# Optimization experiments

Hardware: AMD Instinct MI355X
Metric: run time of the kernel (lower is better)

The kernel has to match this reference:

```python
import jax, jax.numpy as jnp
import numpy as np

B, S, D, E, K = 4, 4096, 1024, 8, 2


def setup_inputs() -> dict:
    key = jax.random.key(0)
    k0, k1, k2 = jax.random.split(key, 3)
    return {
        "x": jax.random.normal(k0, (B, S, D), dtype=jnp.float32),
        "gate_w": jax.random.normal(k1, (E, D), dtype=jnp.float32) * 0.02,   # torch Linear weight [out,in]
        "gate_b": jnp.zeros((E,), dtype=jnp.float32),
        "expert_w": jax.random.normal(k2, (E, D, D), dtype=jnp.float32) * 0.02,  # [E, out, in]
        "expert_b": jnp.zeros((E, D), dtype=jnp.float32),
    }


def reference(x, gate_w, gate_b, expert_w, expert_b):
    b, s, d = x.shape
    h = x.reshape(-1, d)                                   # [T, D], T = b*s
    # Router: gate linear -> softmax (float32) -> top-k -> renormalize
    router_logits = h @ gate_w.T + gate_b                  # [T, E]
    probs = jax.nn.softmax(router_logits.astype(jnp.float32), axis=-1)
    router_weights, selected_experts = jax.lax.top_k(probs, K)  # [T, K]
    router_weights = router_weights / router_weights.sum(axis=-1, keepdims=True)
    router_weights = router_weights.astype(h.dtype)
    # Combine weights per (token, expert): sum of top-k weights routed to each expert
    cw = (jax.nn.one_hot(selected_experts, E, dtype=h.dtype)
          * router_weights[..., None]).sum(axis=1)         # [T, E]
    # Dense-equivalent of gather-linear-scatter: every expert on every token,
    # then weighted combine (mathematically identical to the per-expert loop).
    expert_out = jnp.einsum('td,eod->teo', h, expert_w) + expert_b[None]  # [T, E, D]
    out = jnp.einsum('te,teo->to', cw, expert_out)         # [T, D]
    return out.reshape(b, s, d), router_logits, selected_experts
```

## Files before the change

kernel.cpp:

```cpp
#include <hip/hip_runtime.h>
#include <hip/hip_bf16.h>

#define T_TOK 16384
#define D_DIM 1024
#define E_EXP 8
#define NPAIR 28

#define BM 128
#define BN 128
#define BK 64

#define CNT_STRIDE 64

typedef __attribute__((ext_vector_type(4))) float f32x4;
typedef __attribute__((ext_vector_type(2))) float f32x2;
typedef __attribute__((ext_vector_type(8))) short bf16x8;
typedef __attribute__((ext_vector_type(4))) unsigned short u16x4;

static __device__ __forceinline__ unsigned short f2bf(float f) {
    unsigned int u = __float_as_uint(f);
    unsigned int r = 0x7FFFu + ((u >> 16) & 1u);
    return (unsigned short)((u + r) >> 16);
}

#define GLOAD_LDS16(gp, lp) \
    __builtin_amdgcn_global_load_lds( \
        (const __attribute__((address_space(1))) void*)(gp), \
        (__attribute__((address_space(3))) void*)(lp), 16, 0, 0)

#define RTOK 64
#define RBLK 256
#define CBLK 128
__global__ __launch_bounds__(512) void fused_router_kernel(
    const float* __restrict__ x, const float* __restrict__ gate_w,
    const float* __restrict__ gate_b, float* __restrict__ out_logits,
    float* __restrict__ out_sel, int* __restrict__ counts,
    int* __restrict__ pair_token, f32x2* __restrict__ pair_w,
    unsigned short* __restrict__ xbf,
    const float* __restrict__ expert_w, unsigned short* __restrict__ wbf) {
    const int tid = threadIdx.x;
    if (blockIdx.x >= RBLK) {
        const int b = blockIdx.x - RBLK;
        const int n4 = (E_EXP * D_DIM * D_DIM) / 4;
        for (int i = b * 512 + tid; i < n4; i += CBLK * 512) {
            f32x4 v = ((const f32x4*)expert_w)[i];
            u16x4 p;
            p[0] = f2bf(v[0]); p[1] = f2bf(v[1]); p[2] = f2bf(v[2]); p[3] = f2bf(v[3]);
            ((u16x4*)wbf)[i] = p;
        }
        return;
    }
    __shared__ float gw[E_EXP][D_DIM];
    __shared__ float gb_s[E_EXP];
    __shared__ float logits_s[RTOK][E_EXP];
    __shared__ int   cnt_local[NPAIR];
    __shared__ int   gbase[NPAIR];
    __shared__ int   ent_p[RTOK];
    __shared__ int   ent_pos[RTOK];
    __shared__ f32x2 ent_w[RTOK];

    for (int i = tid; i < E_EXP * D_DIM; i += 512) gw[0][i] = gate_w[i];
    if (tid < E_EXP) gb_s[tid] = gate_b[tid];
    if (tid < NPAIR) cnt_local[tid] = 0;
    __syncthreads();

    const int lane = tid & 63, wv = tid >> 6;
    for (int j = 0; j < RTOK / 8; ++j) {
        const int jt = wv * (RTOK / 8) + j;
        const int t = blockIdx.x * RTOK + jt;
        const float* xrow = x + (size_t)t * D_DIM;
        unsigned short* xbrow = xbf + (size_t)t * D_DIM;
        float acc[E_EXP] = {};
        #pragma unroll
        for (int c = 0; c < 4; ++c) {
            const int col = c * 256 + lane * 4;
            f32x4 xv = *(const f32x4*)(xrow + col);
            u16x4 pk;
            pk[0] = f2bf(xv[0]); pk[1] = f2bf(xv[1]); pk[2] = f2bf(xv[2]); pk[3] = f2bf(xv[3]);
            *(u16x4*)(xbrow + col) = pk;
            #pragma unroll
            for (int e = 0; e < E_EXP; ++e) {
                f32x4 gv = *(const f32x4*)(&gw[e][col]);
                acc[e] += xv[0] * gv[0] + xv[1] * gv[1] + xv[2] * gv[2] + xv[3] * gv[3];
            }
        }
        #pragma unroll
        for (int e = 0; e < E_EXP; ++e) {
            float v = acc[e];
            #pragma unroll
            for (int off = 32; off > 0; off >>= 1) v += __shfl_xor(v, off, 64);
            acc[e] = v;
        }
        if (lane == 0) {
            #pragma unroll
            for (int e = 0; e < E_EXP; ++e) logits_s[jt][e] = acc[e] + gb_s[e];
        }
    }
    __syncthreads();
    if (tid < RTOK) {
        const int t = blockIdx.x * RTOK + tid;
        float l[E_EXP], p[E_EXP];
        float m = -1e30f;
        #pragma unroll
        for (int e = 0; e < E_EXP; ++e) { l[e] = logits_s[tid][e]; m = fmaxf(m, l[e]); }
        float s = 0.f;
        #pragma unroll
        for (int e = 0; e < E_EXP; ++e) { p[e] = expf(l[e] - m); s += p[e]; }
        #pragma unroll
        for (int e = 0; e < E_EXP; ++e) p[e] /= s;
        int e0 = 0; float p0 = p[0];
        #pragma unroll
        for (int e = 1; e < E_EXP; ++e) if (p[e] > p0) { p0 = p[e]; e0 = e; }
        int e1 = -1; float p1 = -1e30f;
        #pragma unroll
        for (int e = 0; e < E_EXP; ++e) if (e != e0 && p[e] > p1) { p1 = p[e]; e1 = e; }
        float denom = p0 + p1;
        float w0 = p0 / denom, w1 = p1 / denom;
        out_sel[t * 2 + 0] = (float)e0;
        out_sel[t * 2 + 1] = (float)e1;
        int lo = min(e0, e1), hi = max(e0, e1);
        float wl = (e0 < e1) ? w0 : w1;
        float wh = (e0 < e1) ? w1 : w0;
        int pp = (lo * (15 - lo)) / 2 + (hi - lo - 1);
        int pos = atomicAdd(&cnt_local[pp], 1);
        ent_p[tid] = pp; ent_pos[tid] = pos;
        f32x2 wv2; wv2[0] = wl; wv2[1] = wh;
        ent_w[tid] = wv2;
    }
    __syncthreads();
    if (tid < NPAIR) gbase[tid] = atomicAdd(&counts[tid * CNT_STRIDE], cnt_local[tid]);
    if (tid < RTOK * E_EXP / 4) {
        f32x4 v = ((const f32x4*)&logits_s[0][0])[tid];
        ((f32x4*)(out_logits + (size_t)blockIdx.x * RTOK * E_EXP))[tid] = v;
    }
    __syncthreads();
    if (tid < RTOK) {
        int pp = ent_p[tid];
        int pos = gbase[pp] + ent_pos[tid];
        pair_token[pp * T_TOK + pos] = blockIdx.x * RTOK + tid;
        pair_w[pp * T_TOK + pos] = ent_w[tid];
    }
}

__global__ __launch_bounds__(256, 2) void moe_gemm_kernel(
    const unsigned short* __restrict__ xbf, const unsigned short* __restrict__ wbf,
    const float* __restrict__ expert_b, const int* __restrict__ counts,
    const int* __restrict__ pair_token, const f32x2* __restrict__ pair_w,
    float* __restrict__ out) {
    const int flat = blockIdx.x;
    const int cls = flat & 7;
    const int nt  = (flat >> 3) & 7;
    const int sup = flat >> 6;
    const int gidx = sup * 8 + cls;

    __shared__ int hdr[5];
    const int tid = threadIdx.x;
    if (tid < 64) {
        int c = (tid < NPAIR) ? counts[tid * CNT_STRIDE] : 0;
        int ntp = (c + BM - 1) >> 7;
        int s = ntp;
        #pragma unroll
        for (int off = 1; off < 64; off <<= 1) {
            int v = __shfl_up(s, off, 64);
            if (tid >= off) s += v;
        }
        int excl = s - ntp;
        bool mine = (tid < NPAIR) && (gidx >= excl) && (gidx < s);
        unsigned long long mb = __ballot(mine);
        int p = mb ? (__ffsll((long long)mb) - 1) : 0;
        int exclp = __shfl(excl, p, 64);
        int cp = __shfl(c, p, 64);
        if (tid == 0) {
            if (mb == 0) { hdr[0] = -1; }
            else {
                int lo = 0, q = p;
                while (q >= 7 - lo) { q -= 7 - lo; ++lo; }
                hdr[0] = lo; hdr[1] = lo + 1 + q;
                hdr[2] = (gidx - exclp) * BM; hdr[3] = cp; hdr[4] = p;
            }
        }
    }
    __syncthreads();
    const int lo = hdr[0];
    if (lo < 0) return;
    const int hi = hdr[1];
    const int m_base = hdr[2];
    const int cnt = hdr[3];
    const int p = hdr[4];
    const int n_base = nt * BN;

    __shared__ unsigned short As[BM * BK];
    __shared__ unsigned short B0s[BM * BK];
    __shared__ unsigned short B1s[BM * BK];
    __shared__ int tok_s[BM];
    __shared__ f32x2 w_s[BM];

    if (tid < BM) {
        int m = m_base + tid;
        int mc = (m < cnt) ? m : (cnt - 1);
        tok_s[tid] = pair_token[p * T_TOK + mc];
        w_s[tid]   = pair_w[p * T_TOK + mc];
    }
    __syncthreads();

    const int lane = tid & 63;
    const int w = tid >> 6;
    const int lr = lane & 15, lk = lane >> 4;
    const int wr = w >> 1, wc = w & 1;

    const int srow = lane >> 3;
    const int scol = 8 * ((lane & 7) ^ srow);
    const unsigned short* wb0 = wbf + ((size_t)lo << 20);
    const unsigned short* wb1 = wbf + ((size_t)hi << 20);
    const unsigned short* agp[4];
    const unsigned short* b0gp[4];
    const unsigned short* b1gp[4];
    int loff[4];
    #pragma unroll
    for (int i = 0; i < 4; ++i) {
        int R = i * 32 + w * 8 + srow;
        agp[i]  = xbf + (size_t)tok_s[R] * D_DIM + scol;
        b0gp[i] = wb0 + (size_t)(n_base + R) * D_DIM + scol;
        b1gp[i] = wb1 + (size_t)(n_base + R) * D_DIM + scol;
        loff[i] = (i * 32 + w * 8) * BK;
    }

    f32x4 acc0[4][4] = {};
    f32x4 acc1[4][4] = {};

    for (int k0 = 0; k0 < D_DIM; k0 += BK) {
        #pragma unroll
        for (int i = 0; i < 4; ++i) {
            GLOAD_LDS16(agp[i] + k0, &As[loff[i]]);
            GLOAD_LDS16(b0gp[i] + k0, &B0s[loff[i]]);
            GLOAD_LDS16(b1gp[i] + k0, &B1s[loff[i]]);
        }
        __syncthreads();
        #pragma unroll
        for (int kk = 0; kk < 2; ++kk) {
            bf16x8 a[4], b[4], c[4];
            #pragma unroll
            for (int m = 0; m < 4; ++m) {
                int R = wr * 64 + m * 16 + lr;
                int cb = (kk * 64 + lk * 16) ^ ((R & 7) << 4);
                a[m] = *(const bf16x8*)((const char*)As + R * 128 + cb);
            }
            #pragma unroll
            for (int n = 0; n < 4; ++n) {
                int R = wc * 64 + n * 16 + lr;
                int cb = (kk * 64 + lk * 16) ^ ((R & 7) << 4);
                b[n] = *(const bf16x8*)((const char*)B0s + R * 128 + cb);
            }
            #pragma unroll
            for (int m = 0; m < 4; ++m)
                #pragma unroll
                for (int n = 0; n < 4; ++n)
                    acc0[m][n] = __builtin_amdgcn_mfma_f32_16x16x32_bf16(a[m], b[n], acc0[m][n], 0, 0, 0);
            #pragma unroll
            for (int n = 0; n < 4; ++n) {
                int R = wc * 64 + n * 16 + lr;
                int cb = (kk * 64 + lk * 16) ^ ((R & 7) << 4);
                c[n] = *(const bf16x8*)((const char*)B1s + R * 128 + cb);
            }
            #pragma unroll
            for (int m = 0; m < 4; ++m)
                #pragma unroll
                for (int n = 0; n < 4; ++n)
                    acc1[m][n] = __builtin_amdgcn_mfma_f32_16x16x32_bf16(a[m], c[n], acc1[m][n], 0, 0, 0);
        }
        __syncthreads();
    }

    float blo[4], bhi[4];
    #pragma unroll
    for (int n = 0; n < 4; ++n) {
        int gn = n_base + wc * 64 + n * 16 + lr;
        blo[n] = expert_b[lo * D_DIM + gn];
        bhi[n] = expert_b[hi * D_DIM + gn];
    }
    #pragma unroll
    for (int m = 0; m < 4; ++m) {
        #pragma unroll
        for (int j = 0; j < 4; ++j) {
            int mi = wr * 64 + m * 16 + lk * 4 + j;
            if (m_base + mi >= cnt) continue;
            int tk = tok_s[mi];
            f32x2 wgt = w_s[mi];
            size_t obase = (size_t)tk * D_DIM + n_base + wc * 64 + lr;
            #pragma unroll
            for (int n = 0; n < 4; ++n)
                out[obase + n * 16] = wgt[0] * (acc0[m][n][j] + blo[n])
                                    + wgt[1] * (acc1[m][n][j] + bhi[n]);
        }
    }
}

extern "C" void kernel_launch(void* const* d_in, const int* in_sizes, int n_in,
                              void* d_out, int out_size, void* d_ws, size_t ws_size,
                              hipStream_t stream) {
    const float* x        = (const float*)d_in[0];
    const float* gate_w   = (const float*)d_in[1];
    const float* gate_b   = (const float*)d_in[2];
    const float* expert_w = (const float*)d_in[3];
    const float* expert_b = (const float*)d_in[4];

    float* out        = (float*)d_out;
    float* out_logits = out + (size_t)T_TOK * D_DIM;
    float* out_sel    = out_logits + (size_t)T_TOK * E_EXP;

    char* ws = (char*)d_ws;
    unsigned short* wbf = (unsigned short*)ws;
    unsigned short* xbf = (unsigned short*)(ws + 16777216);
    size_t off = 50331648;
    int*   counts     = (int*)(ws + off);
    int*   pair_token = (int*)(ws + off + 16384);
    f32x2* pair_w     = (f32x2*)(ws + off + 16384 + 1835008);

    hipMemsetAsync(counts, 0, NPAIR * CNT_STRIDE * sizeof(int), stream);

    fused_router_kernel<<<RBLK + CBLK, 512, 0, stream>>>(
        x, gate_w, gate_b, out_logits, out_sel, counts, pair_token, pair_w,
        xbf, expert_w, wbf);
    moe_gemm_kernel<<<20 * 64, 256, 0, stream>>>(xbf, wbf, expert_b, counts,
                                                 pair_token, pair_w, out);
}
```

Before: 135.2 us.

## Halve N tile to 64 and remap tile index to contiguous chunks per XCD class

Shrinks the output N tile from 128 to 64, which doubles the grid (2560 blocks) and cuts per-block accumulators, LDS and register use. The tile-to-pair mapping changes so that each XCD class takes a contiguous chunk of the M-tile range computed from the total tile count, replacing the strided sup*8+cls layout. The goals are better CU occupancy and load balance, plus keeping gathered token rows local to one XCD cache. In exchange, A tiles are loaded twice as often for the same output and the MFMA work per load drops.

```diff
diff --git a/kernel.cpp b/kernel.cpp
--- a/kernel.cpp
+++ b/kernel.cpp
@@ -7,7 +7,7 @@
 #define NPAIR 28
 
 #define BM 128
-#define BN 128
+#define BN 64
 #define BK 64
 
 #define CNT_STRIDE 64
@@ -149,9 +149,8 @@
     float* __restrict__ out) {
     const int flat = blockIdx.x;
     const int cls = flat & 7;
-    const int nt  = (flat >> 3) & 7;
-    const int sup = flat >> 6;
-    const int gidx = sup * 8 + cls;
+    const int nt  = (flat >> 3) & 15;
+    const int sup = flat >> 7;
 
     __shared__ int hdr[5];
     const int tid = threadIdx.x;
@@ -165,7 +164,11 @@
             if (tid >= off) s += v;
         }
         int excl = s - ntp;
-        bool mine = (tid < NPAIR) && (gidx >= excl) && (gidx < s);
+        int ntot = __shfl(s, NPAIR - 1, 64);
+        int chunk = (ntot + 7) >> 3;
+        int gidx = cls * chunk + sup;
+        bool valid = (sup < chunk) && (gidx < ntot);
+        bool mine = valid && (tid < NPAIR) && (gidx >= excl) && (gidx < s);
         unsigned long long mb = __ballot(mine);
         int p = mb ? (__ffsll((long long)mb) - 1) : 0;
         int exclp = __shfl(excl, p, 64);
@@ -190,8 +193,8 @@
     const int n_base = nt * BN;
 
     __shared__ unsigned short As[BM * BK];
-    __shared__ unsigned short B0s[BM * BK];
-    __shared__ unsigned short B1s[BM * BK];
+    __shared__ unsigned short B0s[BN * BK];
+    __shared__ unsigned short B1s[BN * BK];
     __shared__ int tok_s[BM];
     __shared__ f32x2 w_s[BM];
 
@@ -206,75 +209,76 @@
     const int lane = tid & 63;
     const int w = tid >> 6;
     const int lr = lane & 15, lk = lane >> 4;
-    const int wr = w >> 1, wc = w & 1;
+    const int wm = w >> 1, wn = w & 1;
 
     const int srow = lane >> 3;
     const int scol = 8 * ((lane & 7) ^ srow);
     const unsigned short* wb0 = wbf + ((size_t)lo << 20);
     const unsigned short* wb1 = wbf + ((size_t)hi << 20);
     const unsigned short* agp[4];
-    const unsigned short* b0gp[4];
-    const unsigned short* b1gp[4];
-    int loff[4];
+    const unsigned short* b0gp[2];
+    const unsigned short* b1gp[2];
+    int loffA[4], loffB[2];
     #pragma unroll
     for (int i = 0; i < 4; ++i) {
         int R = i * 32 + w * 8 + srow;
         agp[i]  = xbf + (size_t)tok_s[R] * D_DIM + scol;
+        loffA[i] = (i * 32 + w * 8) * BK;
+    }
+    #pragma unroll
+    for (int i = 0; i < 2; ++i) {
+        int R = i * 32 + w * 8 + srow;
         b0gp[i] = wb0 + (size_t)(n_base + R) * D_DIM + scol;
         b1gp[i] = wb1 + (size_t)(n_base + R) * D_DIM + scol;
-        loff[i] = (i * 32 + w * 8) * BK;
-    }
-
-    f32x4 acc0[4][4] = {};
-    f32x4 acc1[4][4] = {};
+        loffB[i] = (i * 32 + w * 8) * BK;
+    }
+
+    f32x4 acc0[4][2] = {};
+    f32x4 acc1[4][2] = {};
 
     for (int k0 = 0; k0 < D_DIM; k0 += BK) {
         #pragma unroll
-        for (int i = 0; i < 4; ++i) {
-            GLOAD_LDS16(agp[i] + k0, &As[loff[i]]);
-            GLOAD_LDS16(b0gp[i] + k0, &B0s[loff[i]]);
-            GLOAD_LDS16(b1gp[i] + k0, &B1s[loff[i]]);
+        for (int i = 0; i < 4; ++i) GLOAD_LDS16(agp[i] + k0, &As[loffA[i]]);
+        #pragma unroll
+        for (int i = 0; i < 2; ++i) {
+            GLOAD_LDS16(b0gp[i] + k0, &B0s[loffB[i]]);
+            GLOAD_LDS16(b1gp[i] + k0, &B1s[loffB[i]]);
         }
         __syncthreads();
         #pragma unroll
         for (int kk = 0; kk < 2; ++kk) {
-            bf16x8 a[4], b[4], c[4];
+            bf16x8 a[4], b[2], c[2];
             #pragma unroll
             for (int m = 0; m < 4; ++m) {
-                int R = wr * 64 + m * 16 + lr;
+                int R = wm * 64 + m * 16 + lr;
                 int cb = (kk * 64 + lk * 16) ^ ((R & 7) << 4);
                 a[m] = *(const bf16x8*)((const char*)As + R * 128 + cb);
             }
             #pragma unroll
-            for (int n = 0; n < 4; ++n) {
-                int R = wc * 64 + n * 16 + lr;
+            for (int n = 0; n < 2; ++n) {
+                int R = wn * 32 + n * 16 + lr;
                 int cb = (kk * 64 + lk * 16) ^ ((R & 7) << 4);
                 b[n] = *(const bf16x8*)((const char*)B0s + R * 128 + cb);
+                c[n] = *(const bf16x8*)((const char*)B1s + R * 128 + cb);
             }
             #pragma unroll
             for (int m = 0; m < 4; ++m)
                 #pragma unroll
-                for (int n = 0; n < 4; ++n)
+                for (int n = 0; n < 2; ++n)
                     acc0[m][n] = __builtin_amdgcn_mfma_f32_16x16x32_bf16(a[m], b[n], acc0[m][n], 0, 0, 0);
-            #pragma unroll
-            for (int n = 0; n < 4; ++n) {
-                int R = wc * 64 + n * 16 + lr;
-                int cb = (kk * 64 + lk * 16) ^ ((R & 7) << 4);
-                c[n] = *(const bf16x8*)((const char*)B1s + R * 128 + cb);
-            }
             #pragma unroll
             for (int m = 0; m < 4; ++m)
                 #pragma unroll
-                for (int n = 0; n < 4; ++n)
+                for (int n = 0; n < 2; ++n)
                     acc1[m][n] = __builtin_amdgcn_mfma_f32_16x16x32_bf16(a[m], c[n], acc1[m][n], 0, 0, 0);
         }
         __syncthreads();
     }
 
-    float blo[4], bhi[4];
+    float blo[2], bhi[2];
     #pragma unroll
-    for (int n = 0; n < 4; ++n) {
-        int gn = n_base + wc * 64 + n * 16 + lr;
+    for (int n = 0; n < 2; ++n) {
+        int gn = n_base + wn * 32 + n * 16 + lr;
         blo[n] = expert_b[lo * D_DIM + gn];
         bhi[n] = expert_b[hi * D_DIM + gn];
     }
@@ -282,13 +286,13 @@
     for (int m = 0; m < 4; ++m) {
         #pragma unroll
         for (int j = 0; j < 4; ++j) {
-            int mi = wr * 64 + m * 16 + lk * 4 + j;
+            int mi = wm * 64 + m * 16 + lk * 4 + j;
             if (m_base + mi >= cnt) continue;
             int tk = tok_s[mi];
             f32x2 wgt = w_s[mi];
-            size_t obase = (size_t)tk * D_DIM + n_base + wc * 64 + lr;
-            #pragma unroll
-            for (int n = 0; n < 4; ++n)
+            size_t obase = (size_t)tk * D_DIM + n_base + wn * 32 + lr;
+            #pragma unroll
+            for (int n = 0; n < 2; ++n)
                 out[obase + n * 16] = wgt[0] * (acc0[m][n][j] + blo[n])
                                     + wgt[1] * (acc1[m][n][j] + bhi[n]);
         }
@@ -321,6 +325,6 @@
     fused_router_kernel<<<RBLK + CBLK, 512, 0, stream>>>(
         x, gate_w, gate_b, out_logits, out_sel, counts, pair_token, pair_w,
         xbf, expert_w, wbf);
-    moe_gemm_kernel<<<20 * 64, 256, 0, stream>>>(xbf, wbf, expert_b, counts,
-                                                 pair_token, pair_w, out);
+    moe_gemm_kernel<<<20 * 16 * 8, 256, 0, stream>>>(xbf, wbf, expert_b, counts,
+                                                     pair_token, pair_w, out);
 }
```

Measured after the change: 130.6 us (median of 2 runs). 3.4% less time.

## Halve K tile to 32 and remap M-tiles to blocks in contiguous chunks

Applied to the files above, without the earlier changes.

The GEMM K tile shrinks from 64 to 32, which halves LDS use per block and adds a new XOR swizzle and load mapping for the 64-byte rows. With less LDS per block, more blocks may fit on each CU, but the kernel now runs twice as many barrier-separated iterations with fewer MFMAs between syncs. Block-to-tile assignment also changes: the flat grid index now assigns each of 8 classes a contiguous chunk of the total M-tile count, which changes the scheduling order and L2 reuse of weight tiles. The launch size stays at 1280 blocks.

```diff
diff --git a/kernel.cpp b/kernel.cpp
--- a/kernel.cpp
+++ b/kernel.cpp
@@ -8,7 +8,7 @@
 
 #define BM 128
 #define BN 128
-#define BK 64
+#define BK 32
 
 #define CNT_STRIDE 64
 
@@ -151,7 +151,6 @@
     const int cls = flat & 7;
     const int nt  = (flat >> 3) & 7;
     const int sup = flat >> 6;
-    const int gidx = sup * 8 + cls;
 
     __shared__ int hdr[5];
     const int tid = threadIdx.x;
@@ -165,7 +164,11 @@
             if (tid >= off) s += v;
         }
         int excl = s - ntp;
-        bool mine = (tid < NPAIR) && (gidx >= excl) && (gidx < s);
+        int ntot = __shfl(s, NPAIR - 1, 64);
+        int chunk = (ntot + 7) >> 3;
+        int gidx = cls * chunk + sup;
+        bool valid = (sup < chunk) && (gidx < ntot);
+        bool mine = valid && (tid < NPAIR) && (gidx >= excl) && (gidx < s);
         unsigned long long mb = __ballot(mine);
         int p = mb ? (__ffsll((long long)mb) - 1) : 0;
         int exclp = __shfl(excl, p, 64);
@@ -190,8 +193,8 @@
     const int n_base = nt * BN;
 
     __shared__ unsigned short As[BM * BK];
-    __shared__ unsigned short B0s[BM * BK];
-    __shared__ unsigned short B1s[BM * BK];
+    __shared__ unsigned short B0s[BN * BK];
+    __shared__ unsigned short B1s[BN * BK];
     __shared__ int tok_s[BM];
     __shared__ f32x2 w_s[BM];
 
@@ -207,22 +210,23 @@
     const int w = tid >> 6;
     const int lr = lane & 15, lk = lane >> 4;
     const int wr = w >> 1, wc = w & 1;
-
-    const int srow = lane >> 3;
-    const int scol = 8 * ((lane & 7) ^ srow);
+    const int jsw = 8 * (lk ^ ((lr >> 1) & 3));
+
+    const int srow = tid >> 2;
+    const int scol = 8 * ((tid & 3) ^ ((srow >> 1) & 3));
     const unsigned short* wb0 = wbf + ((size_t)lo << 20);
     const unsigned short* wb1 = wbf + ((size_t)hi << 20);
-    const unsigned short* agp[4];
-    const unsigned short* b0gp[4];
-    const unsigned short* b1gp[4];
-    int loff[4];
+    const unsigned short* agp[2];
+    const unsigned short* b0gp[2];
+    const unsigned short* b1gp[2];
+    int loff[2];
     #pragma unroll
-    for (int i = 0; i < 4; ++i) {
-        int R = i * 32 + w * 8 + srow;
+    for (int i = 0; i < 2; ++i) {
+        int R = i * 64 + srow;
         agp[i]  = xbf + (size_t)tok_s[R] * D_DIM + scol;
         b0gp[i] = wb0 + (size_t)(n_base + R) * D_DIM + scol;
         b1gp[i] = wb1 + (size_t)(n_base + R) * D_DIM + scol;
-        loff[i] = (i * 32 + w * 8) * BK;
+        loff[i] = (i * 64 + w * 16) * BK;
     }
 
     f32x4 acc0[4][4] = {};
@@ -230,44 +234,31 @@
 
     for (int k0 = 0; k0 < D_DIM; k0 += BK) {
         #pragma unroll
-        for (int i = 0; i < 4; ++i) {
+        for (int i = 0; i < 2; ++i) {
             GLOAD_LDS16(agp[i] + k0, &As[loff[i]]);
             GLOAD_LDS16(b0gp[i] + k0, &B0s[loff[i]]);
             GLOAD_LDS16(b1gp[i] + k0, &B1s[loff[i]]);
         }
         __syncthreads();
-        #pragma unroll
-        for (int kk = 0; kk < 2; ++kk) {
-            bf16x8 a[4], b[4], c[4];
-            #pragma unroll
-            for (int m = 0; m < 4; ++m) {
-                int R = wr * 64 + m * 16 + lr;
-                int cb = (kk * 64 + lk * 16) ^ ((R & 7) << 4);
-                a[m] = *(const bf16x8*)((const char*)As + R * 128 + cb);
-            }
-            #pragma unroll
-            for (int n = 0; n < 4; ++n) {
-                int R = wc * 64 + n * 16 + lr;
-                int cb = (kk * 64 + lk * 16) ^ ((R & 7) << 4);
-                b[n] = *(const bf16x8*)((const char*)B0s + R * 128 + cb);
-            }
-            #pragma unroll
-            for (int m = 0; m < 4; ++m)
-                #pragma unroll
-                for (int n = 0; n < 4; ++n)
-                    acc0[m][n] = __builtin_amdgcn_mfma_f32_16x16x32_bf16(a[m], b[n], acc0[m][n], 0, 0, 0);
-            #pragma unroll
-            for (int n = 0; n < 4; ++n) {
-                int R = wc * 64 + n * 16 + lr;
-                int cb = (kk * 64 + lk * 16) ^ ((R & 7) << 4);
-                c[n] = *(const bf16x8*)((const char*)B1s + R * 128 + cb);
-            }
-            #pragma unroll
-            for (int m = 0; m < 4; ++m)
-                #pragma unroll
-                for (int n = 0; n < 4; ++n)
-                    acc1[m][n] = __builtin_amdgcn_mfma_f32_16x16x32_bf16(a[m], c[n], acc1[m][n], 0, 0, 0);
-        }
+        bf16x8 a[4], b[4], c[4];
+        #pragma unroll
+        for (int m = 0; m < 4; ++m)
+            a[m] = *(const bf16x8*)&As[(wr * 64 + m * 16 + lr) * BK + jsw];
+        #pragma unroll
+        for (int n = 0; n < 4; ++n) {
+            b[n] = *(const bf16x8*)&B0s[(wc * 64 + n * 16 + lr) * BK + jsw];
+            c[n] = *(const bf16x8*)&B1s[(wc * 64 + n * 16 + lr) * BK + jsw];
+        }
+        #pragma unroll
+        for (int m = 0; m < 4; ++m)
+            #pragma unroll
+            for (int n = 0; n < 4; ++n)
+                acc0[m][n] = __builtin_amdgcn_mfma_f32_16x16x32_bf16(a[m], b[n], acc0[m][n], 0, 0, 0);
+        #pragma unroll
+        for (int m = 0; m < 4; ++m)
+            #pragma unroll
+            for (int n = 0; n < 4; ++n)
+                acc1[m][n] = __builtin_amdgcn_mfma_f32_16x16x32_bf16(a[m], c[n], acc1[m][n], 0, 0, 0);
         __syncthreads();
     }
 
@@ -321,6 +312,6 @@
     fused_router_kernel<<<RBLK + CBLK, 512, 0, stream>>>(
         x, gate_w, gate_b, out_logits, out_sel, counts, pair_token, pair_w,
         xbf, expert_w, wbf);
-    moe_gemm_kernel<<<20 * 64, 256, 0, stream>>>(xbf, wbf, expert_b, counts,
-                                                 pair_token, pair_w, out);
+    moe_gemm_kernel<<<20 * 8 * 8, 256, 0, stream>>>(xbf, wbf, expert_b, counts,
+                                                    pair_token, pair_w, out);
 }
```

Result: slower. 149.1 us (+10.2%).
